# Kernel tuning notes

Hardware: AMD Instinct MI355X
Metric: run time of the kernel (lower is better)

## Reference

```python
import jax, jax.numpy as jnp
import numpy as np
import math

HIDDEN = 1024
HEADS = 16
HEAD_DIM = HIDDEN // HEADS
B, S = 4, 2048


def setup_inputs() -> dict:
    key = jax.random.key(0)
    ks = jax.random.split(key, 10)
    scale = 1.0 / math.sqrt(HIDDEN)
    inp = {
        "x": jax.random.normal(ks[0], (B, S, HIDDEN), dtype=jnp.float32),
        "attention_mask": jnp.ones((B, 1, 1, S), dtype=jnp.int32),
        "Wq": jax.random.normal(ks[1], (HIDDEN, HIDDEN), dtype=jnp.float32) * scale,
        "bq": jnp.zeros((HIDDEN,), dtype=jnp.float32),
        "Wk": jax.random.normal(ks[2], (HIDDEN, HIDDEN), dtype=jnp.float32) * scale,
        "bk": jnp.zeros((HIDDEN,), dtype=jnp.float32),
        "Wv": jax.random.normal(ks[3], (HIDDEN, HIDDEN), dtype=jnp.float32) * scale,
        "bv": jnp.zeros((HIDDEN,), dtype=jnp.float32),
        "Wo": jax.random.normal(ks[4], (HIDDEN, HIDDEN), dtype=jnp.float32) * scale,
        "bo": jnp.zeros((HIDDEN,), dtype=jnp.float32),
    }
    return inp


def reference(x, attention_mask, Wq, bq, Wk, bk, Wv, bv, Wo, bo):
    b, s, d = x.shape
    # nn.Linear: x @ W.T + b
    q = (x @ Wq.T + bq).reshape(b, s, HEADS, HEAD_DIM).transpose(0, 2, 1, 3)
    k = (x @ Wk.T + bk).reshape(b, s, HEADS, HEAD_DIM).transpose(0, 2, 1, 3)
    v = (x @ Wv.T + bv).reshape(b, s, HEADS, HEAD_DIM).transpose(0, 2, 1, 3)
    # explicit O(S^2) score matrix, as in the original
    scores = jnp.einsum("bhqd,bhkd->bhqk", q, k) / math.sqrt(HEAD_DIM)
    scores = jnp.where(attention_mask == 0, jnp.float32(-1e9), scores)
    attn = jax.nn.softmax(scores, axis=-1)
    # dropout(p=0.1) treated as identity (eval mode) for a deterministic reference
    out = jnp.einsum("bhqk,bhkd->bhqd", attn, v)
    out = out.transpose(0, 2, 1, 3).reshape(b, s, d)
    return out @ Wo.T + bo
```

## Files before the change

kernel.cpp:

```cpp
#include <hip/hip_runtime.h>
#include <math.h>

#define HID 1024
#define NH  16
#define HD  64
#define NB  4
#define SL  2048
#define MROWS (NB * SL)

typedef __attribute__((ext_vector_type(8))) short short8;
typedef __attribute__((ext_vector_type(4))) float f32x4;
typedef unsigned short ushort_t;
typedef unsigned int uint_t;

__device__ __forceinline__ uint_t f2bf(float x) {
    union { float f; uint_t u; } a; a.f = x;
    return (a.u + 0x7fffu + ((a.u >> 16) & 1u)) >> 16;
}

__device__ __forceinline__ void load_lds16(const void* g, void* l) {
    __builtin_amdgcn_global_load_lds(
        (const __attribute__((address_space(1))) void*)g,
        (__attribute__((address_space(3))) void*)l, 16, 0, 0);
}

__device__ __forceinline__ void gemm_core_bk64(
    const ushort_t* __restrict__ A, const ushort_t* __restrict__ B,
    const int m0, const int n0, ushort_t* As, ushort_t* Bs, f32x4 (&acc)[4][4])
{
    const int tid = threadIdx.x;
    const int w = tid >> 6, lane = tid & 63;
    const int wm = (w & 1) << 6, wn = (w >> 1) << 6;
    const int c = lane & 15, quad = lane >> 4;

    for (int k0 = 0; k0 < HID; k0 += 64) {
        __syncthreads();
        #pragma unroll
        for (int rd = 0; rd < 4; ++rd) {
            const int g = rd * 4 + w;
            const int idx = g * 64 + lane;
            const int r = idx >> 3, sc = idx & 7;
            const int dc = sc ^ (r & 7);
            load_lds16(&A[(size_t)(m0 + r) * HID + k0 + dc * 8], As + g * 512);
            load_lds16(&B[(size_t)(n0 + r) * HID + k0 + dc * 8], Bs + g * 512);
        }
        __syncthreads();

        #pragma unroll
        for (int ks = 0; ks < 2; ++ks) {
            short8 af[4], bf[4];
            #pragma unroll
            for (int i = 0; i < 4; ++i) {
                const int ra = wm + i * 16 + c;
                const int rb = wn + i * 16 + c;
                af[i] = *(const short8*)
                    &As[ra * 64 + ((((ks << 2) + quad) ^ (c & 7)) << 3)];
                bf[i] = *(const short8*)
                    &Bs[rb * 64 + ((((ks << 2) + quad) ^ (c & 7)) << 3)];
            }
            #pragma unroll
            for (int i = 0; i < 4; ++i)
                #pragma unroll
                for (int j = 0; j < 4; ++j)
                    acc[i][j] = __builtin_amdgcn_mfma_f32_16x16x32_bf16(
                        af[i], bf[j], acc[i][j], 0, 0, 0);
        }
    }
}

__global__ __launch_bounds__(256) void cvt_bf16_kernel(
    const float* __restrict__ x,
    const float* __restrict__ wq, const float* __restrict__ wk,
    const float* __restrict__ wv, const float* __restrict__ wo,
    ushort_t* __restrict__ xb, ushort_t* __restrict__ wqb,
    ushort_t* __restrict__ wkb, ushort_t* __restrict__ wvb,
    ushort_t* __restrict__ wob)
{
    const int seg = blockIdx.y;
    const float* src; ushort_t* dst;
    if (seg < 8)       { src = x + (size_t)seg * 1048576; dst = xb + (size_t)seg * 1048576; }
    else if (seg == 8) { src = wq; dst = wqb; }
    else if (seg == 9) { src = wk; dst = wkb; }
    else if (seg == 10){ src = wv; dst = wvb; }
    else               { src = wo; dst = wob; }
    const int i = (blockIdx.x * 256 + threadIdx.x) * 8;
    const float4 a = *(const float4*)&src[i];
    const float4 b = *(const float4*)&src[i + 4];
    uint4 o;
    o.x = f2bf(a.x) | (f2bf(a.y) << 16);
    o.y = f2bf(a.z) | (f2bf(a.w) << 16);
    o.z = f2bf(b.x) | (f2bf(b.y) << 16);
    o.w = f2bf(b.z) | (f2bf(b.w) << 16);
    *(uint4*)&dst[i] = o;
}

__global__ __launch_bounds__(256) void qkv_mfma_kernel(
    const ushort_t* __restrict__ xb,
    const ushort_t* __restrict__ wqb, const ushort_t* __restrict__ wkb,
    const ushort_t* __restrict__ wvb,
    const float* __restrict__ bq, const float* __restrict__ bk,
    const float* __restrict__ bv,
    ushort_t* __restrict__ qo, ushort_t* __restrict__ ko,
    ushort_t* __restrict__ vo)
{
    __shared__ __align__(16) ushort_t As[128 * 64];
    __shared__ __align__(16) ushort_t Bs[128 * 64];

    const int wsel = blockIdx.z;
    const ushort_t* W    = (wsel == 0) ? wqb : (wsel == 1) ? wkb : wvb;
    const float*    bias = (wsel == 0) ? bq  : (wsel == 1) ? bk  : bv;
    const int m0 = blockIdx.y * 128, n0 = blockIdx.x * 128;

    f32x4 acc[4][4];
    const f32x4 zero = {0.f, 0.f, 0.f, 0.f};
    #pragma unroll
    for (int i = 0; i < 4; ++i)
        #pragma unroll
        for (int j = 0; j < 4; ++j) acc[i][j] = zero;

    gemm_core_bk64(xb, W, m0, n0, As, Bs, acc);

    const int tid = threadIdx.x;
    const int w = tid >> 6, lane = tid & 63;
    const int wm = (w & 1) << 6, wn = (w >> 1) << 6;
    const int c = lane & 15, quad = lane >> 4;
    const float qscale = (wsel == 0) ? 0.18033688f : 1.0f;

    #pragma unroll
    for (int j = 0; j < 4; ++j) {
        const int n_g = n0 + wn + j * 16 + c;
        const float bj = bias[n_g];
        const int h = n_g >> 6, d = n_g & 63;
        #pragma unroll
        for (int i = 0; i < 4; ++i) {
            const int mbase = m0 + wm + i * 16 + quad * 4;
            const int b = mbase >> 11;
            const int sbase = mbase & (SL - 1);
            if (wsel == 2) {
                ushort4 pk;
                pk.x = (ushort_t)f2bf(acc[i][j][0] + bj);
                pk.y = (ushort_t)f2bf(acc[i][j][1] + bj);
                pk.z = (ushort_t)f2bf(acc[i][j][2] + bj);
                pk.w = (ushort_t)f2bf(acc[i][j][3] + bj);
                *(ushort4*)&vo[(((size_t)(b * NH + h) * HD) + d) * SL + sbase] = pk;
            } else {
                ushort_t* dst = (wsel == 0) ? qo : ko;
                #pragma unroll
                for (int reg = 0; reg < 4; ++reg) {
                    const float v = (acc[i][j][reg] + bj) * qscale;
                    dst[(((size_t)(b * NH + h) * SL) + sbase + reg) * HD + d] =
                        (ushort_t)f2bf(v);
                }
            }
        }
    }
}

__global__ __launch_bounds__(256, 4) void attn_mfma_kernel(
    const ushort_t* __restrict__ q, const ushort_t* __restrict__ k,
    const ushort_t* __restrict__ vt, const int* __restrict__ mask,
    ushort_t* __restrict__ ao)
{
    __shared__ __align__(16) ushort_t Ks[64 * 64];
    __shared__ __align__(16) ushort_t Vs[64 * 64];
    __shared__ __align__(16) ushort_t Ps[128 * 72];

    const int qt = blockIdx.x;
    const int bh = blockIdx.y;
    const int b = bh >> 4, h = bh & 15;
    const int tid = threadIdx.x;
    const int w = tid >> 6, lane = tid & 63;
    const int c = lane & 15, quad = lane >> 4;

    const ushort_t* qp = q  + (size_t)bh * SL * HD + (size_t)qt * 128 * HD;
    const ushort_t* kp = k  + (size_t)bh * SL * HD;
    const ushort_t* vp = vt + (size_t)bh * HD * SL;

    short8 qf[2][2];
    #pragma unroll
    for (int mi = 0; mi < 2; ++mi)
        #pragma unroll
        for (int ks = 0; ks < 2; ++ks)
            qf[mi][ks] = *(const short8*)&qp[(size_t)(w * 32 + mi * 16 + c) * HD
                                             + ks * 32 + quad * 8];

    float l_s[2][4] = {};
    f32x4 oa[2][4];
    const f32x4 zero = {0.f, 0.f, 0.f, 0.f};
    #pragma unroll
    for (int mi = 0; mi < 2; ++mi)
        #pragma unroll
        for (int ni = 0; ni < 4; ++ni) oa[mi][ni] = zero;

    for (int kt = 0; kt < SL / 64; ++kt) {
        __syncthreads();
        #pragma unroll
        for (int rd = 0; rd < 2; ++rd) {
            const int g = rd * 4 + w;
            const int t = g * 64 + lane;
            const int r = t >> 3, sc = t & 7;
            const int dck = sc ^ ((r >> 2) & 7);
            const int dcv = sc ^ (r & 7);
            load_lds16(&kp[(size_t)(kt * 64 + r) * HD + dck * 8], Ks + g * 512);
            load_lds16(&vp[(size_t)r * SL + kt * 64 + dcv * 8], Vs + g * 512);
        }
        __syncthreads();

        f32x4 sf[2][4];
        #pragma unroll
        for (int mi = 0; mi < 2; ++mi)
            #pragma unroll
            for (int ni = 0; ni < 4; ++ni) sf[mi][ni] = zero;
        #pragma unroll
        for (int ni = 0; ni < 4; ++ni) {
            const int krow = 4 * c + ni;
            #pragma unroll
            for (int ks = 0; ks < 2; ++ks) {
                const short8 kf = *(const short8*)
                    &Ks[krow * 64 + (((ks * 4 + quad) ^ (c & 7)) << 3)];
                #pragma unroll
                for (int mi = 0; mi < 2; ++mi)
                    sf[mi][ni] = __builtin_amdgcn_mfma_f32_16x16x32_bf16(
                        qf[mi][ks], kf, sf[mi][ni], 0, 0, 0);
            }
        }

        const int4 mzv = *(const int4*)&mask[b * SL + kt * 64 + 4 * c];
        const int mz[4] = {mzv.x, mzv.y, mzv.z, mzv.w};

        #pragma unroll
        for (int mi = 0; mi < 2; ++mi) {
            #pragma unroll
            for (int reg = 0; reg < 4; ++reg) {
                float p[4];
                #pragma unroll
                for (int ni = 0; ni < 4; ++ni) {
                    float pv = __builtin_amdgcn_exp2f(sf[mi][ni][reg]);
                    p[ni] = (mz[ni] == 0) ? 0.f : pv;
                }
                l_s[mi][reg] += (p[0] + p[1]) + (p[2] + p[3]);
                union { float f; uint_t u; } u0, u1, u2, u3;
                u0.f = p[0]; u1.f = p[1]; u2.f = p[2]; u3.f = p[3];
                uint2 pk;
                pk.x = __builtin_amdgcn_perm(u1.u, u0.u, 0x07060302u);
                pk.y = __builtin_amdgcn_perm(u3.u, u2.u, 0x07060302u);
                *(uint2*)&Ps[(w * 32 + mi * 16 + quad * 4 + reg) * 72 + 4 * c] = pk;
            }
        }

        short8 pf[2][2];
        #pragma unroll
        for (int mi = 0; mi < 2; ++mi)
            #pragma unroll
            for (int ks = 0; ks < 2; ++ks)
                pf[mi][ks] = *(const short8*)
                    &Ps[(w * 32 + mi * 16 + c) * 72 + ks * 32 + quad * 8];
        #pragma unroll
        for (int ni = 0; ni < 4; ++ni) {
            const int n = ni * 16 + c;
            #pragma unroll
            for (int ks = 0; ks < 2; ++ks) {
                const short8 vf = *(const short8*)
                    &Vs[n * 64 + (((ks * 4 + quad) ^ (c & 7)) << 3)];
                #pragma unroll
                for (int mi = 0; mi < 2; ++mi)
                    oa[mi][ni] = __builtin_amdgcn_mfma_f32_16x16x32_bf16(
                        pf[mi][ks], vf, oa[mi][ni], 0, 0, 0);
            }
        }
    }

    #pragma unroll
    for (int mi = 0; mi < 2; ++mi) {
        #pragma unroll
        for (int reg = 0; reg < 4; ++reg) {
            float l = l_s[mi][reg];
            #pragma unroll
            for (int off = 1; off < 16; off <<= 1)
                l += __shfl_xor(l, off, 64);
            const float inv = 1.f / l;
            const int s_g = qt * 128 + w * 32 + mi * 16 + quad * 4 + reg;
            #pragma unroll
            for (int ni = 0; ni < 4; ++ni) {
                const int d = ni * 16 + c;
                ao[((size_t)(b * SL + s_g)) * HID + h * HD + d] =
                    (ushort_t)f2bf(oa[mi][ni][reg] * inv);
            }
        }
    }
}

__global__ __launch_bounds__(256) void out_mfma_kernel(
    const ushort_t* __restrict__ aob, const ushort_t* __restrict__ wob,
    const float* __restrict__ bo, float* __restrict__ out)
{
    __shared__ __align__(16) ushort_t As[128 * 64];
    __shared__ __align__(16) ushort_t Bs[128 * 64];

    const int m0 = blockIdx.y * 128, n0 = blockIdx.x * 128;

    f32x4 acc[4][4];
    const f32x4 zero = {0.f, 0.f, 0.f, 0.f};
    #pragma unroll
    for (int i = 0; i < 4; ++i)
        #pragma unroll
        for (int j = 0; j < 4; ++j) acc[i][j] = zero;

    gemm_core_bk64(aob, wob, m0, n0, As, Bs, acc);

    const int tid = threadIdx.x;
    const int w = tid >> 6, lane = tid & 63;
    const int wm = (w & 1) << 6, wn = (w >> 1) << 6;
    const int c = lane & 15, quad = lane >> 4;

    #pragma unroll
    for (int j = 0; j < 4; ++j) {
        const int n_g = n0 + wn + j * 16 + c;
        const float bj = bo[n_g];
        #pragma unroll
        for (int i = 0; i < 4; ++i) {
            const int mbase = m0 + wm + i * 16 + quad * 4;
            #pragma unroll
            for (int reg = 0; reg < 4; ++reg)
                out[(size_t)(mbase + reg) * HID + n_g] = acc[i][j][reg] + bj;
        }
    }
}

extern "C" void kernel_launch(void* const* d_in, const int* in_sizes, int n_in,
                              void* d_out, int out_size, void* d_ws, size_t ws_size,
                              hipStream_t stream)
{
    const float* x    = (const float*)d_in[0];
    const int*   mask = (const int*)d_in[1];
    const float* Wq   = (const float*)d_in[2];
    const float* bq   = (const float*)d_in[3];
    const float* Wk   = (const float*)d_in[4];
    const float* bk   = (const float*)d_in[5];
    const float* Wv   = (const float*)d_in[6];
    const float* bv   = (const float*)d_in[7];
    const float* Wo   = (const float*)d_in[8];
    const float* bo   = (const float*)d_in[9];
    float* out = (float*)d_out;

    ushort_t* p = (ushort_t*)d_ws;
    ushort_t* xb  = p; p += (size_t)MROWS * HID;
    ushort_t* wqb = p; p += (size_t)HID * HID;
    ushort_t* wkb = p; p += (size_t)HID * HID;
    ushort_t* wvb = p; p += (size_t)HID * HID;
    ushort_t* wob = p; p += (size_t)HID * HID;
    ushort_t* qb  = p; p += (size_t)MROWS * HID;
    ushort_t* kb  = p; p += (size_t)MROWS * HID;
    ushort_t* vtb = p; p += (size_t)MROWS * HID;
    ushort_t* aob = p; p += (size_t)MROWS * HID;

    cvt_bf16_kernel<<<dim3(512, 12), 256, 0, stream>>>(
        x, Wq, Wk, Wv, Wo, xb, wqb, wkb, wvb, wob);
    qkv_mfma_kernel<<<dim3(8, 64, 3), 256, 0, stream>>>(
        xb, wqb, wkb, wvb, bq, bk, bv, qb, kb, vtb);
    attn_mfma_kernel<<<dim3(16, 64), 256, 0, stream>>>(
        qb, kb, vtb, mask, aob);
    out_mfma_kernel<<<dim3(8, 64), 256, 0, stream>>>(
        aob, wob, bo, out);
}
```

Measured before the change: 293.9 us.

## Register-prefetch next K/V tile and XOR-swizzle P buffer in attention

Replaces the direct global-to-LDS loads of the K and V tiles with register prefetching: the next tile is loaded into registers during the current tile's compute, then written to swizzled LDS at the top of the next iteration. The padded P staging buffer (stride 72) becomes an XOR-swizzled stride-64 layout, which cuts LDS use, and launch bounds are raised to 5 blocks per SM for more occupancy. The aim is to hide global load latency behind the MFMA work and fit more blocks per CU. The cost is extra VGPRs for the prefetch buffers under a tighter register budget, which may cause spills.

```diff
diff --git a/kernel.cpp b/kernel.cpp
--- a/kernel.cpp
+++ b/kernel.cpp
@@ -156,14 +156,14 @@
     }
 }
 
-__global__ __launch_bounds__(256, 4) void attn_mfma_kernel(
+__global__ __launch_bounds__(256, 5) void attn_mfma_kernel(
     const ushort_t* __restrict__ q, const ushort_t* __restrict__ k,
     const ushort_t* __restrict__ vt, const int* __restrict__ mask,
     ushort_t* __restrict__ ao)
 {
     __shared__ __align__(16) ushort_t Ks[64 * 64];
     __shared__ __align__(16) ushort_t Vs[64 * 64];
-    __shared__ __align__(16) ushort_t Ps[128 * 72];
+    __shared__ __align__(16) ushort_t Ps[128 * 64];
 
     const int qt = blockIdx.x;
     const int bh = blockIdx.y;
@@ -192,19 +192,35 @@
         #pragma unroll
         for (int ni = 0; ni < 4; ++ni) oa[mi][ni] = zero;
 
+    uint4 kr[2], vr[2];
+    #pragma unroll
+    for (int rd = 0; rd < 2; ++rd) {
+        const int t = (rd * 4 + w) * 64 + lane;
+        const int r = t >> 3, sc = t & 7;
+        kr[rd] = *(const uint4*)&kp[(size_t)r * HD + sc * 8];
+        vr[rd] = *(const uint4*)&vp[(size_t)r * SL + sc * 8];
+    }
+
     for (int kt = 0; kt < SL / 64; ++kt) {
         __syncthreads();
         #pragma unroll
         for (int rd = 0; rd < 2; ++rd) {
-            const int g = rd * 4 + w;
-            const int t = g * 64 + lane;
+            const int t = (rd * 4 + w) * 64 + lane;
             const int r = t >> 3, sc = t & 7;
-            const int dck = sc ^ ((r >> 2) & 7);
-            const int dcv = sc ^ (r & 7);
-            load_lds16(&kp[(size_t)(kt * 64 + r) * HD + dck * 8], Ks + g * 512);
-            load_lds16(&vp[(size_t)r * SL + kt * 64 + dcv * 8], Vs + g * 512);
+            *(uint4*)&Ks[(r * 8 + (sc ^ ((r >> 2) & 7))) * 8] = kr[rd];
+            *(uint4*)&Vs[(r * 8 + (sc ^ (r & 7))) * 8] = vr[rd];
         }
         __syncthreads();
+
+        if (kt + 1 < SL / 64) {
+            #pragma unroll
+            for (int rd = 0; rd < 2; ++rd) {
+                const int t = (rd * 4 + w) * 64 + lane;
+                const int r = t >> 3, sc = t & 7;
+                kr[rd] = *(const uint4*)&kp[(size_t)((kt + 1) * 64 + r) * HD + sc * 8];
+                vr[rd] = *(const uint4*)&vp[(size_t)r * SL + (kt + 1) * 64 + sc * 8];
+            }
+        }
 
         f32x4 sf[2][4];
         #pragma unroll
@@ -244,7 +260,9 @@
                 uint2 pk;
                 pk.x = __builtin_amdgcn_perm(u1.u, u0.u, 0x07060302u);
                 pk.y = __builtin_amdgcn_perm(u3.u, u2.u, 0x07060302u);
-                *(uint2*)&Ps[(w * 32 + mi * 16 + quad * 4 + reg) * 72 + 4 * c] = pk;
+                const int prow = w * 32 + mi * 16 + quad * 4 + reg;
+                *(uint2*)&Ps[prow * 64 + (((c >> 1) ^ (prow & 7)) * 8)
+                             + ((c & 1) * 4)] = pk;
             }
         }
 
@@ -252,9 +270,11 @@
         #pragma unroll
         for (int mi = 0; mi < 2; ++mi)
             #pragma unroll
-            for (int ks = 0; ks < 2; ++ks)
+            for (int ks = 0; ks < 2; ++ks) {
+                const int prow = w * 32 + mi * 16 + c;
                 pf[mi][ks] = *(const short8*)
-                    &Ps[(w * 32 + mi * 16 + c) * 72 + ks * 32 + quad * 8];
+                    &Ps[prow * 64 + (((ks * 4 + quad) ^ (prow & 7)) << 3)];
+            }
         #pragma unroll
         for (int ni = 0; ni < 4; ++ni) {
             const int n = ni * 16 + c;
```

After: 559.8 us. +90.5%, slower.
